# Optimization experiments

Hardware: AMD Instinct MI355X
Metric: run time of the kernel (lower is better)

## Reference

```python
import jax, jax.numpy as jnp
import numpy as np

N = 100000   # nodes
E = 1600000  # edges (avg degree 16)
D = 128      # input feature dim
H = 128      # Config.hidden_dim
G = 64       # graphs in batch
OUT = 2      # output classes


def setup_inputs() -> dict:
    key = jax.random.key(0)
    ks = jax.random.split(key, 12)
    s = 0.05
    return {
        "x": jax.random.normal(ks[0], (N, D), dtype=jnp.float32),
        "edge_index": jax.random.randint(ks[1], (2, E), 0, N),
        "batch": jnp.sort(jax.random.randint(ks[2], (N,), 0, G)),
        "W1": jax.random.normal(ks[3], (H, D), dtype=jnp.float32) * s,
        "b1": jnp.zeros((H,), jnp.float32),
        "W2": jax.random.normal(ks[4], (H, H), dtype=jnp.float32) * s,
        "b2": jnp.zeros((H,), jnp.float32),
        "Wf1": jax.random.normal(ks[5], (H, H), dtype=jnp.float32) * s,
        "bf1": jnp.zeros((H,), jnp.float32),
        "Wf2": jax.random.normal(ks[6], (OUT, H), dtype=jnp.float32) * s,
        "bf2": jnp.zeros((OUT,), jnp.float32),
    }


def _gnn_layer(x, src, dst, W, b):
    # message(x_j) = Linear(x[src]); linear commutes with gather, so transform
    # node features once (N rows) instead of per-edge (E rows): same math.
    xw = x @ W.T + b                                   # [N, H]
    msg = xw[src]                                      # [E, H] gather
    summed = jax.ops.segment_sum(msg, dst, num_segments=N)            # [N, H]
    cnt = jax.ops.segment_sum(jnp.ones((src.shape[0],), x.dtype), dst,
                              num_segments=N)                          # [N]
    return summed / jnp.maximum(cnt, 1.0)[:, None]     # scatter-mean (0 for deg-0)


def reference(x, edge_index, batch, W1, b1, W2, b2, Wf1, bf1, Wf2, bf2):
    src, dst = edge_index[0], edge_index[1]
    h = jax.nn.relu(_gnn_layer(x, src, dst, W1, b1))
    h = jax.nn.relu(_gnn_layer(h, src, dst, W2, b2))
    g = jax.ops.segment_max(h, batch, num_segments=G)  # global_max_pool [G, H]
    z = jax.nn.relu(g @ Wf1.T + bf1)                   # fc (dropout = identity, eval)
    z = z @ Wf2.T + bf2                                # [G, OUT]
    return jax.nn.log_softmax(z, axis=1)
```

## Files before the change

### kernel.cpp

```cpp
#include <hip/hip_runtime.h>
#include <hip/hip_fp16.h>
#include <math.h>


#define SPLIT 16
#define BUCKET_SHIFT 8
#define BUCKET_SIZE 256
#define MAXBUCK 512
#define BIN_CHUNK 4096
#define CAP 4608
#define LSTR 136

typedef _Float16 half8 __attribute__((ext_vector_type(8)));
typedef _Float16 half4v __attribute__((ext_vector_type(4)));
typedef _Float16 half2v __attribute__((ext_vector_type(2)));
typedef float floatx4 __attribute__((ext_vector_type(4)));
typedef float floatx2 __attribute__((ext_vector_type(2)));

__global__ void k_init(int* bcur, int* gstart, int* gend, int G, int nbuck) {
    int i = threadIdx.x;
    if (i < nbuck) bcur[i] = i * CAP;
    if (i < G) { gstart[i] = 0; gend[i] = 0; }
}

__global__ void k_bin(const int* __restrict__ src, const int* __restrict__ dst,
                      int* __restrict__ bcur, int* __restrict__ staging,
                      int E, int nbuck) {
    __shared__ int lh[MAXBUCK];
    __shared__ int lbase[MAXBUCK];
    __shared__ int lc[MAXBUCK];
    for (int i = threadIdx.x; i < nbuck; i += blockDim.x) { lh[i] = 0; lc[i] = 0; }
    __syncthreads();
    int base = blockIdx.x * BIN_CHUNK;
    int end = min(base + BIN_CHUNK, E);
    for (int e = base + threadIdx.x; e < end; e += blockDim.x)
        atomicAdd(&lh[dst[e] >> BUCKET_SHIFT], 1);
    __syncthreads();
    for (int i = threadIdx.x; i < nbuck; i += blockDim.x)
        if (lh[i]) lbase[i] = atomicAdd(&bcur[i], lh[i]);
    __syncthreads();
    for (int e = base + threadIdx.x; e < end; e += blockDim.x) {
        int d = dst[e];
        int b = d >> BUCKET_SHIFT;
        int pos = lbase[b] + atomicAdd(&lc[b], 1);
        if (pos < (b + 1) * CAP)
            staging[pos] = src[e] | ((d & (BUCKET_SIZE - 1)) << 24);
    }
}

__global__ __launch_bounds__(BUCKET_SIZE) void k_bcsr(
        const int* __restrict__ staging, const int* __restrict__ bcur,
        int* __restrict__ esrc, int* __restrict__ rowstart,
        int* __restrict__ deg, int N) {
    __shared__ int lh[BUCKET_SIZE];
    __shared__ int lrs[BUCKET_SIZE];
    __shared__ int lcur[BUCKET_SIZE];
    int b = blockIdx.x;
    int s = b * CAP;
    int e = min(bcur[b], s + CAP);
    int t = threadIdx.x;
    lh[t] = 0;
    __syncthreads();
    for (int i = s + t; i < e; i += BUCKET_SIZE)
        atomicAdd(&lh[((unsigned)staging[i]) >> 24], 1);
    __syncthreads();
    int v = lh[t];
    lrs[t] = v;
    __syncthreads();
    for (int off = 1; off < BUCKET_SIZE; off <<= 1) {
        int x = (t >= off) ? lrs[t - off] : 0;
        __syncthreads();
        lrs[t] += x;
        __syncthreads();
    }
    int excl = lrs[t] - v;
    int node = b * BUCKET_SIZE + t;
    if (node < N) { rowstart[node] = s + excl; deg[node] = v; }
    lcur[t] = excl;
    __syncthreads();
    for (int i = s + t; i < e; i += BUCKET_SIZE) {
        int p = staging[i];
        int local = ((unsigned)p) >> 24;
        int pos = atomicAdd(&lcur[local], 1);
        esrc[s + pos] = p & 0xFFFFFF;
    }
}

template <typename T>
__global__ __launch_bounds__(512) void k_gemm(const T* __restrict__ in,
                                              const float* __restrict__ W,
                                              const float* __restrict__ bias,
                                              unsigned char* __restrict__ out8,
                                              int N) {
    __shared__ _Float16 sX[128 * LSTR];
    __shared__ _Float16 sW[128 * LSTR];
    int t = threadIdx.x;
    int n0 = blockIdx.x * 128;

    #pragma unroll
    for (int it = 0; it < 8; ++it) {
        int lin = it * 512 + t;
        int r = lin >> 5;
        int c = (lin & 31) * 4;
        half4v xh;
        int n = n0 + r;
        if (n < N) {
            if constexpr (sizeof(T) == 4) {
                float4 xv = *(const float4*)((const float*)in + (size_t)n * 128 + c);
                xh = half4v{ (_Float16)xv.x, (_Float16)xv.y, (_Float16)xv.z, (_Float16)xv.w };
            } else {
                xh = *(const half4v*)((const _Float16*)in + (size_t)n * 128 + c);
            }
        } else {
            xh = half4v{ 0, 0, 0, 0 };
        }
        float4 wv = *(const float4*)(W + r * 128 + c);
        half4v wh = { (_Float16)wv.x, (_Float16)wv.y, (_Float16)wv.z, (_Float16)wv.w };
        *(half4v*)&sX[r * LSTR + c] = xh;
        *(half4v*)&sW[r * LSTR + c] = wh;
    }
    __syncthreads();

    int w = t >> 6;
    int lane = t & 63;
    int quad = lane >> 4;
    int lrow = lane & 15;

    floatx4 acc[8];
    #pragma unroll
    for (int i = 0; i < 8; ++i) acc[i] = {0.f, 0.f, 0.f, 0.f};

    int arow = (w * 16 + lrow) * LSTR + quad * 8;
    #pragma unroll
    for (int k0 = 0; k0 < 128; k0 += 32) {
        half8 a = *(const half8*)&sX[arow + k0];
        #pragma unroll
        for (int ht = 0; ht < 8; ++ht) {
            half8 b = *(const half8*)&sW[(ht * 16 + lrow) * LSTR + quad * 8 + k0];
            acc[ht] = __builtin_amdgcn_mfma_f32_16x16x32_f16(a, b, acc[ht], 0, 0, 0);
        }
    }

    #pragma unroll
    for (int ht = 0; ht < 8; ++ht) {
        int h = ht * 16 + lrow;
        float bv = bias[h];
        #pragma unroll
        for (int r = 0; r < 4; ++r) {
            int node = n0 + w * 16 + quad * 4 + r;
            if (node < N) {
                float v = acc[ht][r] + bv;
                int pk = __builtin_amdgcn_cvt_pk_fp8_f32(v, v, 0, false);
                out8[(size_t)node * 128 + h] = (unsigned char)(pk & 0xFF);
            }
        }
    }
}

__global__ __launch_bounds__(256) void k_agg(const unsigned char* __restrict__ in8,
                                             const int* __restrict__ esrc,
                                             const int* __restrict__ rowstart,
                                             const int* __restrict__ deg,
                                             _Float16* __restrict__ outh, int N) {
    int lane = threadIdx.x & 63;
    int node = blockIdx.x * 4 + (threadIdx.x >> 6);
    if (node >= N) return;
    int start = __builtin_amdgcn_readfirstlane(rowstart[node]);
    int d     = __builtin_amdgcn_readfirstlane(deg[node]);
    const unsigned short* in16 = (const unsigned short*)in8;

    floatx2 a0 = {0.f, 0.f}, a1 = {0.f, 0.f}, a2 = {0.f, 0.f}, a3 = {0.f, 0.f};

    int i = 0;
    for (; i + 8 <= d; i += 8) {
        int x0 = __builtin_amdgcn_readfirstlane(esrc[start + i + 0]);
        int x1 = __builtin_amdgcn_readfirstlane(esrc[start + i + 1]);
        int x2 = __builtin_amdgcn_readfirstlane(esrc[start + i + 2]);
        int x3 = __builtin_amdgcn_readfirstlane(esrc[start + i + 3]);
        int x4 = __builtin_amdgcn_readfirstlane(esrc[start + i + 4]);
        int x5 = __builtin_amdgcn_readfirstlane(esrc[start + i + 5]);
        int x6 = __builtin_amdgcn_readfirstlane(esrc[start + i + 6]);
        int x7 = __builtin_amdgcn_readfirstlane(esrc[start + i + 7]);
        unsigned u0 = in16[((size_t)x0 << 6) + lane];
        unsigned u1 = in16[((size_t)x1 << 6) + lane];
        unsigned u2 = in16[((size_t)x2 << 6) + lane];
        unsigned u3 = in16[((size_t)x3 << 6) + lane];
        unsigned u4 = in16[((size_t)x4 << 6) + lane];
        unsigned u5 = in16[((size_t)x5 << 6) + lane];
        unsigned u6 = in16[((size_t)x6 << 6) + lane];
        unsigned u7 = in16[((size_t)x7 << 6) + lane];
        floatx2 f0 = __builtin_amdgcn_cvt_pk_f32_fp8(u0, false);
        floatx2 f1 = __builtin_amdgcn_cvt_pk_f32_fp8(u1, false);
        floatx2 f2 = __builtin_amdgcn_cvt_pk_f32_fp8(u2, false);
        floatx2 f3 = __builtin_amdgcn_cvt_pk_f32_fp8(u3, false);
        floatx2 f4 = __builtin_amdgcn_cvt_pk_f32_fp8(u4, false);
        floatx2 f5 = __builtin_amdgcn_cvt_pk_f32_fp8(u5, false);
        floatx2 f6 = __builtin_amdgcn_cvt_pk_f32_fp8(u6, false);
        floatx2 f7 = __builtin_amdgcn_cvt_pk_f32_fp8(u7, false);
        a0.x += f0.x; a0.y += f0.y;  a1.x += f1.x; a1.y += f1.y;
        a2.x += f2.x; a2.y += f2.y;  a3.x += f3.x; a3.y += f3.y;
        a0.x += f4.x; a0.y += f4.y;  a1.x += f5.x; a1.y += f5.y;
        a2.x += f6.x; a2.y += f6.y;  a3.x += f7.x; a3.y += f7.y;
    }
    for (; i + 4 <= d; i += 4) {
        int x0 = __builtin_amdgcn_readfirstlane(esrc[start + i + 0]);
        int x1 = __builtin_amdgcn_readfirstlane(esrc[start + i + 1]);
        int x2 = __builtin_amdgcn_readfirstlane(esrc[start + i + 2]);
        int x3 = __builtin_amdgcn_readfirstlane(esrc[start + i + 3]);
        unsigned u0 = in16[((size_t)x0 << 6) + lane];
        unsigned u1 = in16[((size_t)x1 << 6) + lane];
        unsigned u2 = in16[((size_t)x2 << 6) + lane];
        unsigned u3 = in16[((size_t)x3 << 6) + lane];
        floatx2 f0 = __builtin_amdgcn_cvt_pk_f32_fp8(u0, false);
        floatx2 f1 = __builtin_amdgcn_cvt_pk_f32_fp8(u1, false);
        floatx2 f2 = __builtin_amdgcn_cvt_pk_f32_fp8(u2, false);
        floatx2 f3 = __builtin_amdgcn_cvt_pk_f32_fp8(u3, false);
        a0.x += f0.x; a0.y += f0.y;  a1.x += f1.x; a1.y += f1.y;
        a2.x += f2.x; a2.y += f2.y;  a3.x += f3.x; a3.y += f3.y;
    }
    for (; i < d; ++i) {
        int x0 = __builtin_amdgcn_readfirstlane(esrc[start + i]);
        unsigned u0 = in16[((size_t)x0 << 6) + lane];
        floatx2 f0 = __builtin_amdgcn_cvt_pk_f32_fp8(u0, false);
        a0.x += f0.x; a0.y += f0.y;
    }

    float sx = (a0.x + a1.x) + (a2.x + a3.x);
    float sy = (a0.y + a1.y) + (a2.y + a3.y);
    float dm = fmaxf((float)d, 1.0f);
    half2v r = { (_Float16)fmaxf(sx / dm, 0.f),
                 (_Float16)fmaxf(sy / dm, 0.f) };
    *(half2v*)(outh + (size_t)node * 128 + lane * 2) = r;
}

__global__ void k_bounds(const int* __restrict__ batch, int* __restrict__ gstart,
                         int* __restrict__ gend, int N) {
    int n = blockIdx.x * blockDim.x + threadIdx.x;
    if (n >= N) return;
    int b = batch[n];
    if (n == 0 || batch[n - 1] != b) gstart[b] = n;
    if (n == N - 1 || batch[n + 1] != b) gend[b] = n + 1;
}

__global__ void k_pool1(const _Float16* __restrict__ h, const int* __restrict__ gstart,
                        const int* __restrict__ gend, float* __restrict__ pm, int G) {
    int g = blockIdx.x / SPLIT;
    int c = blockIdx.x % SPLIT;
    int t = threadIdx.x;
    int s = gstart[g], e = gend[g];
    int len = e - s;
    int chunk = (len + SPLIT - 1) / SPLIT;
    int lo = s + c * chunk;
    int hi = min(lo + chunk, e);
    float m = -INFINITY;
    for (int n = lo; n < hi; ++n)
        m = fmaxf(m, (float)h[(size_t)n * 128 + t]);
    pm[((size_t)g * SPLIT + c) * 128 + t] = m;
}

__global__ void k_fc(const float* __restrict__ pm,
                     const float* __restrict__ Wf1, const float* __restrict__ bf1,
                     const float* __restrict__ Wf2, const float* __restrict__ bf2,
                     float* __restrict__ out) {
    __shared__ float sg[128];
    __shared__ float sz[128];
    __shared__ float so[2];
    int g = blockIdx.x;
    int t = threadIdx.x;
    float m = -INFINITY;
    #pragma unroll
    for (int c = 0; c < SPLIT; ++c)
        m = fmaxf(m, pm[((size_t)g * SPLIT + c) * 128 + t]);
    sg[t] = m;
    __syncthreads();
    float z = bf1[t];
    #pragma unroll 4
    for (int d = 0; d < 128; ++d)
        z += sg[d] * Wf1[t * 128 + d];
    sz[t] = fmaxf(z, 0.f);
    __syncthreads();
    if (t < 2) {
        float o = bf2[t];
        for (int d = 0; d < 128; ++d)
            o += sz[d] * Wf2[t * 128 + d];
        so[t] = o;
    }
    __syncthreads();
    if (t == 0) {
        float a = so[0], b = so[1];
        float mx = fmaxf(a, b);
        float ls = mx + logf(expf(a - mx) + expf(b - mx));
        out[g * 2 + 0] = a - ls;
        out[g * 2 + 1] = b - ls;
    }
}

extern "C" void kernel_launch(void* const* d_in, const int* in_sizes, int n_in,
                              void* d_out, int out_size, void* d_ws, size_t ws_size,
                              hipStream_t stream) {
    const float* x   = (const float*)d_in[0];
    const int*   ei  = (const int*)d_in[1];
    const int* batch = (const int*)d_in[2];
    const float* W1  = (const float*)d_in[3];
    const float* b1  = (const float*)d_in[4];
    const float* W2  = (const float*)d_in[5];
    const float* b2  = (const float*)d_in[6];
    const float* Wf1 = (const float*)d_in[7];
    const float* bf1 = (const float*)d_in[8];
    const float* Wf2 = (const float*)d_in[9];
    const float* bf2 = (const float*)d_in[10];

    int N = in_sizes[2];
    int E = in_sizes[1] / 2;
    int G = out_size / 2;
    const int* src = ei;
    const int* dst = ei + E;
    int nbuck = (N + BUCKET_SIZE - 1) / BUCKET_SIZE;

    char* p = (char*)d_ws;
    auto alloc = [&](size_t bytes) -> char* {
        char* r = p;
        p += (bytes + 255) & ~(size_t)255;
        return r;
    };
    unsigned char* A = (unsigned char*)alloc((size_t)N * 128);
    _Float16* B    = (_Float16*)alloc((size_t)N * 128 * 2);
    int* deg       = (int*)alloc((size_t)N * 4);
    int* rowstart  = (int*)alloc((size_t)N * 4);
    int* esrc      = (int*)alloc((size_t)nbuck * CAP * 4);
    int* staging   = (int*)alloc((size_t)nbuck * CAP * 4);
    int* bcur      = (int*)alloc((MAXBUCK + 2) * 4);
    int* gstart    = (int*)alloc((size_t)G * 4);
    int* gend      = (int*)alloc((size_t)G * 4);
    float* pm      = (float*)alloc((size_t)G * SPLIT * 128 * 4);

    int nchunk = (E + BIN_CHUNK - 1) / BIN_CHUNK;

    k_init<<<1, MAXBUCK, 0, stream>>>(bcur, gstart, gend, G, nbuck);
    k_bin<<<nchunk, 256, 0, stream>>>(src, dst, bcur, staging, E, nbuck);
    k_bcsr<<<nbuck, BUCKET_SIZE, 0, stream>>>(staging, bcur, esrc, rowstart, deg, N);
    k_bounds<<<(N + 255) / 256, 256, 0, stream>>>(batch, gstart, gend, N);

    k_gemm<float><<<(N + 127) / 128, 512, 0, stream>>>(x, W1, b1, A, N);
    k_agg<<<(N + 3) / 4, 256, 0, stream>>>(A, esrc, rowstart, deg, B, N);
    k_gemm<_Float16><<<(N + 127) / 128, 512, 0, stream>>>(B, W2, b2, A, N);
    k_agg<<<(N + 3) / 4, 256, 0, stream>>>(A, esrc, rowstart, deg, B, N);
    k_pool1<<<G * SPLIT, 128, 0, stream>>>(B, gstart, gend, pm, G);
    k_fc<<<G, 128, 0, stream>>>(pm, Wf1, bf1, Wf2, bf2, (float*)d_out);
}
```

Baseline: 303.6 us.

## Fuse graph-bounds into binning, vectorize bin loads, use wave-shuffle scan in bucket CSR

Moves the per-graph start/end boundary computation into the edge-binning kernel, removing one kernel launch. The bin kernel now loads each full chunk's src/dst with int4 vector loads once and keeps them in registers, so the second pass no longer reads global memory again. The bucket-CSR prefix sum changes from a shared-memory Hillis-Steele scan with many barriers to a wavefront shuffle scan plus a small cross-wave combine. The cost is more register pressure in the bin kernel and a coverage assumption: the bin grid must have at least N threads for the fused bounds work, which holds for these sizes.

```diff
diff --git a/kernel.cpp b/kernel.cpp
--- a/kernel.cpp
+++ b/kernel.cpp
@@ -17,34 +17,77 @@
 typedef float floatx4 __attribute__((ext_vector_type(4)));
 typedef float floatx2 __attribute__((ext_vector_type(2)));
 
+#define RFL(v) __builtin_amdgcn_readfirstlane(v)
+
 __global__ void k_init(int* bcur, int* gstart, int* gend, int G, int nbuck) {
     int i = threadIdx.x;
     if (i < nbuck) bcur[i] = i * CAP;
     if (i < G) { gstart[i] = 0; gend[i] = 0; }
 }
 
-__global__ void k_bin(const int* __restrict__ src, const int* __restrict__ dst,
-                      int* __restrict__ bcur, int* __restrict__ staging,
-                      int E, int nbuck) {
+__global__ __launch_bounds__(256) void k_bin(
+        const int* __restrict__ src, const int* __restrict__ dst,
+        int* __restrict__ bcur, int* __restrict__ staging,
+        const int* __restrict__ batch, int* __restrict__ gstart,
+        int* __restrict__ gend, int E, int N, int nbuck) {
     __shared__ int lh[MAXBUCK];
     __shared__ int lbase[MAXBUCK];
     __shared__ int lc[MAXBUCK];
-    for (int i = threadIdx.x; i < nbuck; i += blockDim.x) { lh[i] = 0; lc[i] = 0; }
-    __syncthreads();
+    int t = threadIdx.x;
+    for (int i = t; i < nbuck; i += 256) { lh[i] = 0; lc[i] = 0; }
+
+    int n = blockIdx.x * 256 + t;
+    if (n < N) {
+        int b = batch[n];
+        if (n == 0 || batch[n - 1] != b) gstart[b] = n;
+        if (n == N - 1 || batch[n + 1] != b) gend[b] = n + 1;
+    }
+    __syncthreads();
+
     int base = blockIdx.x * BIN_CHUNK;
-    int end = min(base + BIN_CHUNK, E);
-    for (int e = base + threadIdx.x; e < end; e += blockDim.x)
-        atomicAdd(&lh[dst[e] >> BUCKET_SHIFT], 1);
-    __syncthreads();
-    for (int i = threadIdx.x; i < nbuck; i += blockDim.x)
-        if (lh[i]) lbase[i] = atomicAdd(&bcur[i], lh[i]);
-    __syncthreads();
-    for (int e = base + threadIdx.x; e < end; e += blockDim.x) {
-        int d = dst[e];
-        int b = d >> BUCKET_SHIFT;
-        int pos = lbase[b] + atomicAdd(&lc[b], 1);
-        if (pos < (b + 1) * CAP)
-            staging[pos] = src[e] | ((d & (BUCKET_SIZE - 1)) << 24);
+    if (base + BIN_CHUNK <= E) {
+        int ds[16], ss[16];
+        const int4* dv = (const int4*)(dst + base);
+        const int4* sv = (const int4*)(src + base);
+        #pragma unroll
+        for (int j = 0; j < 4; ++j) {
+            int4 d = dv[j * 256 + t];
+            int4 s = sv[j * 256 + t];
+            ds[j * 4 + 0] = d.x; ds[j * 4 + 1] = d.y;
+            ds[j * 4 + 2] = d.z; ds[j * 4 + 3] = d.w;
+            ss[j * 4 + 0] = s.x; ss[j * 4 + 1] = s.y;
+            ss[j * 4 + 2] = s.z; ss[j * 4 + 3] = s.w;
+        }
+        #pragma unroll
+        for (int q = 0; q < 16; ++q)
+            atomicAdd(&lh[ds[q] >> BUCKET_SHIFT], 1);
+        __syncthreads();
+        for (int i = t; i < nbuck; i += 256)
+            if (lh[i]) lbase[i] = atomicAdd(&bcur[i], lh[i]);
+        __syncthreads();
+        #pragma unroll
+        for (int q = 0; q < 16; ++q) {
+            int d = ds[q];
+            int b = d >> BUCKET_SHIFT;
+            int pos = lbase[b] + atomicAdd(&lc[b], 1);
+            if (pos < (b + 1) * CAP)
+                staging[pos] = ss[q] | ((d & (BUCKET_SIZE - 1)) << 24);
+        }
+    } else {
+        int end = E;
+        for (int e = base + t; e < end; e += 256)
+            atomicAdd(&lh[dst[e] >> BUCKET_SHIFT], 1);
+        __syncthreads();
+        for (int i = t; i < nbuck; i += 256)
+            if (lh[i]) lbase[i] = atomicAdd(&bcur[i], lh[i]);
+        __syncthreads();
+        for (int e = base + t; e < end; e += 256) {
+            int d = dst[e];
+            int b = d >> BUCKET_SHIFT;
+            int pos = lbase[b] + atomicAdd(&lc[b], 1);
+            if (pos < (b + 1) * CAP)
+                staging[pos] = src[e] | ((d & (BUCKET_SIZE - 1)) << 24);
+        }
     }
 }
 
@@ -53,8 +96,8 @@
         int* __restrict__ esrc, int* __restrict__ rowstart,
         int* __restrict__ deg, int N) {
     __shared__ int lh[BUCKET_SIZE];
-    __shared__ int lrs[BUCKET_SIZE];
     __shared__ int lcur[BUCKET_SIZE];
+    __shared__ int ws[4];
     int b = blockIdx.x;
     int s = b * CAP;
     int e = min(bcur[b], s + CAP);
@@ -65,15 +108,21 @@
         atomicAdd(&lh[((unsigned)staging[i]) >> 24], 1);
     __syncthreads();
     int v = lh[t];
-    lrs[t] = v;
-    __syncthreads();
-    for (int off = 1; off < BUCKET_SIZE; off <<= 1) {
-        int x = (t >= off) ? lrs[t - off] : 0;
-        __syncthreads();
-        lrs[t] += x;
-        __syncthreads();
-    }
-    int excl = lrs[t] - v;
+    int lane = t & 63;
+    int wv = t >> 6;
+    int inc = v;
+    #pragma unroll
+    for (int off = 1; off < 64; off <<= 1) {
+        int x = __shfl_up(inc, off, 64);
+        if (lane >= off) inc += x;
+    }
+    if (lane == 63) ws[wv] = inc;
+    __syncthreads();
+    int woff = 0;
+    #pragma unroll
+    for (int k = 0; k < 3; ++k)
+        if (k < wv) woff += ws[k];
+    int excl = woff + inc - v;
     int node = b * BUCKET_SIZE + t;
     if (node < N) { rowstart[node] = s + excl; deg[node] = v; }
     lcur[t] = excl;
@@ -165,22 +214,22 @@
     int lane = threadIdx.x & 63;
     int node = blockIdx.x * 4 + (threadIdx.x >> 6);
     if (node >= N) return;
-    int start = __builtin_amdgcn_readfirstlane(rowstart[node]);
-    int d     = __builtin_amdgcn_readfirstlane(deg[node]);
+    int start = RFL(rowstart[node]);
+    int d     = RFL(deg[node]);
     const unsigned short* in16 = (const unsigned short*)in8;
 
     floatx2 a0 = {0.f, 0.f}, a1 = {0.f, 0.f}, a2 = {0.f, 0.f}, a3 = {0.f, 0.f};
 
     int i = 0;
     for (; i + 8 <= d; i += 8) {
-        int x0 = __builtin_amdgcn_readfirstlane(esrc[start + i + 0]);
-        int x1 = __builtin_amdgcn_readfirstlane(esrc[start + i + 1]);
-        int x2 = __builtin_amdgcn_readfirstlane(esrc[start + i + 2]);
-        int x3 = __builtin_amdgcn_readfirstlane(esrc[start + i + 3]);
-        int x4 = __builtin_amdgcn_readfirstlane(esrc[start + i + 4]);
-        int x5 = __builtin_amdgcn_readfirstlane(esrc[start + i + 5]);
-        int x6 = __builtin_amdgcn_readfirstlane(esrc[start + i + 6]);
-        int x7 = __builtin_amdgcn_readfirstlane(esrc[start + i + 7]);
+        int x0 = RFL(esrc[start + i + 0]);
+        int x1 = RFL(esrc[start + i + 1]);
+        int x2 = RFL(esrc[start + i + 2]);
+        int x3 = RFL(esrc[start + i + 3]);
+        int x4 = RFL(esrc[start + i + 4]);
+        int x5 = RFL(esrc[start + i + 5]);
+        int x6 = RFL(esrc[start + i + 6]);
+        int x7 = RFL(esrc[start + i + 7]);
         unsigned u0 = in16[((size_t)x0 << 6) + lane];
         unsigned u1 = in16[((size_t)x1 << 6) + lane];
         unsigned u2 = in16[((size_t)x2 << 6) + lane];
@@ -203,10 +252,10 @@
         a2.x += f6.x; a2.y += f6.y;  a3.x += f7.x; a3.y += f7.y;
     }
     for (; i + 4 <= d; i += 4) {
-        int x0 = __builtin_amdgcn_readfirstlane(esrc[start + i + 0]);
-        int x1 = __builtin_amdgcn_readfirstlane(esrc[start + i + 1]);
-        int x2 = __builtin_amdgcn_readfirstlane(esrc[start + i + 2]);
-        int x3 = __builtin_amdgcn_readfirstlane(esrc[start + i + 3]);
+        int x0 = RFL(esrc[start + i + 0]);
+        int x1 = RFL(esrc[start + i + 1]);
+        int x2 = RFL(esrc[start + i + 2]);
+        int x3 = RFL(esrc[start + i + 3]);
         unsigned u0 = in16[((size_t)x0 << 6) + lane];
         unsigned u1 = in16[((size_t)x1 << 6) + lane];
         unsigned u2 = in16[((size_t)x2 << 6) + lane];
@@ -219,7 +268,7 @@
         a2.x += f2.x; a2.y += f2.y;  a3.x += f3.x; a3.y += f3.y;
     }
     for (; i < d; ++i) {
-        int x0 = __builtin_amdgcn_readfirstlane(esrc[start + i]);
+        int x0 = RFL(esrc[start + i]);
         unsigned u0 = in16[((size_t)x0 << 6) + lane];
         floatx2 f0 = __builtin_amdgcn_cvt_pk_f32_fp8(u0, false);
         a0.x += f0.x; a0.y += f0.y;
@@ -231,15 +280,6 @@
     half2v r = { (_Float16)fmaxf(sx / dm, 0.f),
                  (_Float16)fmaxf(sy / dm, 0.f) };
     *(half2v*)(outh + (size_t)node * 128 + lane * 2) = r;
-}
-
-__global__ void k_bounds(const int* __restrict__ batch, int* __restrict__ gstart,
-                         int* __restrict__ gend, int N) {
-    int n = blockIdx.x * blockDim.x + threadIdx.x;
-    if (n >= N) return;
-    int b = batch[n];
-    if (n == 0 || batch[n - 1] != b) gstart[b] = n;
-    if (n == N - 1 || batch[n + 1] != b) gend[b] = n + 1;
 }
 
 __global__ void k_pool1(const _Float16* __restrict__ h, const int* __restrict__ gstart,
@@ -337,9 +377,9 @@
     int nchunk = (E + BIN_CHUNK - 1) / BIN_CHUNK;
 
     k_init<<<1, MAXBUCK, 0, stream>>>(bcur, gstart, gend, G, nbuck);
-    k_bin<<<nchunk, 256, 0, stream>>>(src, dst, bcur, staging, E, nbuck);
+    k_bin<<<nchunk, 256, 0, stream>>>(src, dst, bcur, staging, batch,
+                                      gstart, gend, E, N, nbuck);
     k_bcsr<<<nbuck, BUCKET_SIZE, 0, stream>>>(staging, bcur, esrc, rowstart, deg, N);
-    k_bounds<<<(N + 255) / 256, 256, 0, stream>>>(batch, gstart, gend, N);
 
     k_gemm<float><<<(N + 127) / 128, 512, 0, stream>>>(x, W1, b1, A, N);
     k_agg<<<(N + 3) / 4, 256, 0, stream>>>(A, esrc, rowstart, deg, B, N);
```

Result: faster. 296.9 us (-2.2%).

## Replace bucketed CSR build with per-node fixed-capacity slots via global atomics

Applied to the files above, without the earlier changes.

Drops the two-pass bucket staging plus local counting sort. Each edge now takes a slot in a fixed 64-entry per-node array through a global atomicAdd on a per-node counter. The batch-boundary detection is folded into the same binning kernel, removing two launches and the staging buffer. The aggregation kernel reads neighbours from node<<6 and divides by the true count, so any edges beyond 64 per destination are silently dropped. It also adds 1.6M returning global atomics and a larger, sparser edge array.

```diff
diff --git a/kernel.cpp b/kernel.cpp
--- a/kernel.cpp
+++ b/kernel.cpp
@@ -4,11 +4,8 @@
 
 
 #define SPLIT 16
-#define BUCKET_SHIFT 8
-#define BUCKET_SIZE 256
-#define MAXBUCK 512
 #define BIN_CHUNK 4096
-#define CAP 4608
+#define NCAP 64
 #define LSTR 136
 
 typedef _Float16 half8 __attribute__((ext_vector_type(8)));
@@ -17,72 +14,52 @@
 typedef float floatx4 __attribute__((ext_vector_type(4)));
 typedef float floatx2 __attribute__((ext_vector_type(2)));
 
-__global__ void k_init(int* bcur, int* gstart, int* gend, int G, int nbuck) {
-    int i = threadIdx.x;
-    if (i < nbuck) bcur[i] = i * CAP;
+#define RFL(v) __builtin_amdgcn_readfirstlane(v)
+
+__global__ void k_init(int* __restrict__ cnt, int* __restrict__ gstart,
+                       int* __restrict__ gend, int N, int G) {
+    int i = blockIdx.x * blockDim.x + threadIdx.x;
+    if (i < N) cnt[i] = 0;
     if (i < G) { gstart[i] = 0; gend[i] = 0; }
 }
 
-__global__ void k_bin(const int* __restrict__ src, const int* __restrict__ dst,
-                      int* __restrict__ bcur, int* __restrict__ staging,
-                      int E, int nbuck) {
-    __shared__ int lh[MAXBUCK];
-    __shared__ int lbase[MAXBUCK];
-    __shared__ int lc[MAXBUCK];
-    for (int i = threadIdx.x; i < nbuck; i += blockDim.x) { lh[i] = 0; lc[i] = 0; }
-    __syncthreads();
+__global__ __launch_bounds__(256) void k_bin2(
+        const int* __restrict__ src, const int* __restrict__ dst,
+        int* __restrict__ cnt, int* __restrict__ esrc,
+        const int* __restrict__ batch, int* __restrict__ gstart,
+        int* __restrict__ gend, int E, int N) {
+    int t = threadIdx.x;
+
+    int n = blockIdx.x * 256 + t;
+    if (n < N) {
+        int b = batch[n];
+        if (n == 0 || batch[n - 1] != b) gstart[b] = n;
+        if (n == N - 1 || batch[n + 1] != b) gend[b] = n + 1;
+    }
+
     int base = blockIdx.x * BIN_CHUNK;
-    int end = min(base + BIN_CHUNK, E);
-    for (int e = base + threadIdx.x; e < end; e += blockDim.x)
-        atomicAdd(&lh[dst[e] >> BUCKET_SHIFT], 1);
-    __syncthreads();
-    for (int i = threadIdx.x; i < nbuck; i += blockDim.x)
-        if (lh[i]) lbase[i] = atomicAdd(&bcur[i], lh[i]);
-    __syncthreads();
-    for (int e = base + threadIdx.x; e < end; e += blockDim.x) {
-        int d = dst[e];
-        int b = d >> BUCKET_SHIFT;
-        int pos = lbase[b] + atomicAdd(&lc[b], 1);
-        if (pos < (b + 1) * CAP)
-            staging[pos] = src[e] | ((d & (BUCKET_SIZE - 1)) << 24);
-    }
-}
-
-__global__ __launch_bounds__(BUCKET_SIZE) void k_bcsr(
-        const int* __restrict__ staging, const int* __restrict__ bcur,
-        int* __restrict__ esrc, int* __restrict__ rowstart,
-        int* __restrict__ deg, int N) {
-    __shared__ int lh[BUCKET_SIZE];
-    __shared__ int lrs[BUCKET_SIZE];
-    __shared__ int lcur[BUCKET_SIZE];
-    int b = blockIdx.x;
-    int s = b * CAP;
-    int e = min(bcur[b], s + CAP);
-    int t = threadIdx.x;
-    lh[t] = 0;
-    __syncthreads();
-    for (int i = s + t; i < e; i += BUCKET_SIZE)
-        atomicAdd(&lh[((unsigned)staging[i]) >> 24], 1);
-    __syncthreads();
-    int v = lh[t];
-    lrs[t] = v;
-    __syncthreads();
-    for (int off = 1; off < BUCKET_SIZE; off <<= 1) {
-        int x = (t >= off) ? lrs[t - off] : 0;
-        __syncthreads();
-        lrs[t] += x;
-        __syncthreads();
-    }
-    int excl = lrs[t] - v;
-    int node = b * BUCKET_SIZE + t;
-    if (node < N) { rowstart[node] = s + excl; deg[node] = v; }
-    lcur[t] = excl;
-    __syncthreads();
-    for (int i = s + t; i < e; i += BUCKET_SIZE) {
-        int p = staging[i];
-        int local = ((unsigned)p) >> 24;
-        int pos = atomicAdd(&lcur[local], 1);
-        esrc[s + pos] = p & 0xFFFFFF;
+    if (base + BIN_CHUNK <= E) {
+        const int4* dv = (const int4*)(dst + base);
+        const int4* sv = (const int4*)(src + base);
+        #pragma unroll
+        for (int j = 0; j < 4; ++j) {
+            int4 d = dv[j * 256 + t];
+            int4 s = sv[j * 256 + t];
+            int p0 = atomicAdd(&cnt[d.x], 1);
+            if (p0 < NCAP) esrc[((size_t)d.x << 6) + p0] = s.x;
+            int p1 = atomicAdd(&cnt[d.y], 1);
+            if (p1 < NCAP) esrc[((size_t)d.y << 6) + p1] = s.y;
+            int p2 = atomicAdd(&cnt[d.z], 1);
+            if (p2 < NCAP) esrc[((size_t)d.z << 6) + p2] = s.z;
+            int p3 = atomicAdd(&cnt[d.w], 1);
+            if (p3 < NCAP) esrc[((size_t)d.w << 6) + p3] = s.w;
+        }
+    } else {
+        for (int e = base + t; e < E; e += 256) {
+            int d = dst[e];
+            int p = atomicAdd(&cnt[d], 1);
+            if (p < NCAP) esrc[((size_t)d << 6) + p] = src[e];
+        }
     }
 }
 
@@ -159,28 +136,28 @@
 
 __global__ __launch_bounds__(256) void k_agg(const unsigned char* __restrict__ in8,
                                              const int* __restrict__ esrc,
-                                             const int* __restrict__ rowstart,
-                                             const int* __restrict__ deg,
+                                             const int* __restrict__ cnt,
                                              _Float16* __restrict__ outh, int N) {
     int lane = threadIdx.x & 63;
     int node = blockIdx.x * 4 + (threadIdx.x >> 6);
     if (node >= N) return;
-    int start = __builtin_amdgcn_readfirstlane(rowstart[node]);
-    int d     = __builtin_amdgcn_readfirstlane(deg[node]);
+    int c  = RFL(cnt[node]);
+    int d  = min(c, NCAP);
+    size_t rb = (size_t)node << 6;
     const unsigned short* in16 = (const unsigned short*)in8;
 
     floatx2 a0 = {0.f, 0.f}, a1 = {0.f, 0.f}, a2 = {0.f, 0.f}, a3 = {0.f, 0.f};
 
     int i = 0;
     for (; i + 8 <= d; i += 8) {
-        int x0 = __builtin_amdgcn_readfirstlane(esrc[start + i + 0]);
-        int x1 = __builtin_amdgcn_readfirstlane(esrc[start + i + 1]);
-        int x2 = __builtin_amdgcn_readfirstlane(esrc[start + i + 2]);
-        int x3 = __builtin_amdgcn_readfirstlane(esrc[start + i + 3]);
-        int x4 = __builtin_amdgcn_readfirstlane(esrc[start + i + 4]);
-        int x5 = __builtin_amdgcn_readfirstlane(esrc[start + i + 5]);
-        int x6 = __builtin_amdgcn_readfirstlane(esrc[start + i + 6]);
-        int x7 = __builtin_amdgcn_readfirstlane(esrc[start + i + 7]);
+        int x0 = RFL(esrc[rb + i + 0]);
+        int x1 = RFL(esrc[rb + i + 1]);
+        int x2 = RFL(esrc[rb + i + 2]);
+        int x3 = RFL(esrc[rb + i + 3]);
+        int x4 = RFL(esrc[rb + i + 4]);
+        int x5 = RFL(esrc[rb + i + 5]);
+        int x6 = RFL(esrc[rb + i + 6]);
+        int x7 = RFL(esrc[rb + i + 7]);
         unsigned u0 = in16[((size_t)x0 << 6) + lane];
         unsigned u1 = in16[((size_t)x1 << 6) + lane];
         unsigned u2 = in16[((size_t)x2 << 6) + lane];
@@ -203,10 +180,10 @@
         a2.x += f6.x; a2.y += f6.y;  a3.x += f7.x; a3.y += f7.y;
     }
     for (; i + 4 <= d; i += 4) {
-        int x0 = __builtin_amdgcn_readfirstlane(esrc[start + i + 0]);
-        int x1 = __builtin_amdgcn_readfirstlane(esrc[start + i + 1]);
-        int x2 = __builtin_amdgcn_readfirstlane(esrc[start + i + 2]);
-        int x3 = __builtin_amdgcn_readfirstlane(esrc[start + i + 3]);
+        int x0 = RFL(esrc[rb + i + 0]);
+        int x1 = RFL(esrc[rb + i + 1]);
+        int x2 = RFL(esrc[rb + i + 2]);
+        int x3 = RFL(esrc[rb + i + 3]);
         unsigned u0 = in16[((size_t)x0 << 6) + lane];
         unsigned u1 = in16[((size_t)x1 << 6) + lane];
         unsigned u2 = in16[((size_t)x2 << 6) + lane];
@@ -219,7 +196,7 @@
         a2.x += f2.x; a2.y += f2.y;  a3.x += f3.x; a3.y += f3.y;
     }
     for (; i < d; ++i) {
-        int x0 = __builtin_amdgcn_readfirstlane(esrc[start + i]);
+        int x0 = RFL(esrc[rb + i]);
         unsigned u0 = in16[((size_t)x0 << 6) + lane];
         floatx2 f0 = __builtin_amdgcn_cvt_pk_f32_fp8(u0, false);
         a0.x += f0.x; a0.y += f0.y;
@@ -227,19 +204,10 @@
 
     float sx = (a0.x + a1.x) + (a2.x + a3.x);
     float sy = (a0.y + a1.y) + (a2.y + a3.y);
-    float dm = fmaxf((float)d, 1.0f);
+    float dm = fmaxf((float)c, 1.0f);
     half2v r = { (_Float16)fmaxf(sx / dm, 0.f),
                  (_Float16)fmaxf(sy / dm, 0.f) };
     *(half2v*)(outh + (size_t)node * 128 + lane * 2) = r;
-}
-
-__global__ void k_bounds(const int* __restrict__ batch, int* __restrict__ gstart,
-                         int* __restrict__ gend, int N) {
-    int n = blockIdx.x * blockDim.x + threadIdx.x;
-    if (n >= N) return;
-    int b = batch[n];
-    if (n == 0 || batch[n - 1] != b) gstart[b] = n;
-    if (n == N - 1 || batch[n + 1] != b) gend[b] = n + 1;
 }
 
 __global__ void k_pool1(const _Float16* __restrict__ h, const int* __restrict__ gstart,
@@ -315,7 +283,6 @@
     int G = out_size / 2;
     const int* src = ei;
     const int* dst = ei + E;
-    int nbuck = (N + BUCKET_SIZE - 1) / BUCKET_SIZE;
 
     char* p = (char*)d_ws;
     auto alloc = [&](size_t bytes) -> char* {
@@ -325,26 +292,22 @@
     };
     unsigned char* A = (unsigned char*)alloc((size_t)N * 128);
     _Float16* B    = (_Float16*)alloc((size_t)N * 128 * 2);
-    int* deg       = (int*)alloc((size_t)N * 4);
-    int* rowstart  = (int*)alloc((size_t)N * 4);
-    int* esrc      = (int*)alloc((size_t)nbuck * CAP * 4);
-    int* staging   = (int*)alloc((size_t)nbuck * CAP * 4);
-    int* bcur      = (int*)alloc((MAXBUCK + 2) * 4);
+    int* cnt       = (int*)alloc((size_t)N * 4);
+    int* esrc      = (int*)alloc((size_t)N * NCAP * 4);
     int* gstart    = (int*)alloc((size_t)G * 4);
     int* gend      = (int*)alloc((size_t)G * 4);
     float* pm      = (float*)alloc((size_t)G * SPLIT * 128 * 4);
 
     int nchunk = (E + BIN_CHUNK - 1) / BIN_CHUNK;
 
-    k_init<<<1, MAXBUCK, 0, stream>>>(bcur, gstart, gend, G, nbuck);
-    k_bin<<<nchunk, 256, 0, stream>>>(src, dst, bcur, staging, E, nbuck);
-    k_bcsr<<<nbuck, BUCKET_SIZE, 0, stream>>>(staging, bcur, esrc, rowstart, deg, N);
-    k_bounds<<<(N + 255) / 256, 256, 0, stream>>>(batch, gstart, gend, N);
+    k_init<<<(N + 255) / 256, 256, 0, stream>>>(cnt, gstart, gend, N, G);
+    k_bin2<<<nchunk, 256, 0, stream>>>(src, dst, cnt, esrc, batch,
+                                       gstart, gend, E, N);
 
     k_gemm<float><<<(N + 127) / 128, 512, 0, stream>>>(x, W1, b1, A, N);
-    k_agg<<<(N + 3) / 4, 256, 0, stream>>>(A, esrc, rowstart, deg, B, N);
+    k_agg<<<(N + 3) / 4, 256, 0, stream>>>(A, esrc, cnt, B, N);
     k_gemm<_Float16><<<(N + 127) / 128, 512, 0, stream>>>(B, W2, b2, A, N);
-    k_agg<<<(N + 3) / 4, 256, 0, stream>>>(A, esrc, rowstart, deg, B, N);
+    k_agg<<<(N + 3) / 4, 256, 0, stream>>>(A, esrc, cnt, B, N);
     k_pool1<<<G * SPLIT, 128, 0, stream>>>(B, gstart, gend, pm, G);
     k_fc<<<G, 128, 0, stream>>>(pm, Wf1, bf1, Wf2, bf2, (float*)d_out);
 }
```

Result: slower. 382.2 us (+25.9%).
